# Optimization experiments

Measured on AMD Instinct MI355X. Metric: run time of the kernel, lower is better.

## Reference

```python
import jax, jax.numpy as jnp
import numpy as np

N = 100_000   # nodes
E = 1_600_000 # edges per relation (avg degree 16)
IN, H, O = 128, 128, 128


def _graph_conv(x, src, dst, W, b, relu):
    """DGL GraphConv, norm='both': y = D_dst^{-1/2} A D_src^{-1/2} x W + b."""
    ones = jnp.ones(src.shape[0], dtype=x.dtype)
    deg_out = jnp.clip(jax.ops.segment_sum(ones, src, num_segments=N), 1.0)  # [N]
    deg_in = jnp.clip(jax.ops.segment_sum(ones, dst, num_segments=N), 1.0)   # [N]
    h = (x * (deg_out ** -0.5)[:, None]) @ W                 # [N, out] transform first (in==out)
    agg = jax.ops.segment_sum(h[src], dst, num_segments=N)   # SpMM: gather + scatter-add
    y = agg * (deg_in ** -0.5)[:, None] + b
    return jax.nn.relu(y) if relu else y


def setup_inputs() -> dict:
    key = jax.random.key(0)
    ks = jax.random.split(key, 8)
    g = 0.1  # weight scale ~ xavier for d=128
    return {
        "x": jax.random.normal(ks[0], (N, IN), dtype=jnp.float32),
        "src_i": jax.random.randint(ks[1], (E,), 0, N),
        "dst_i": jax.random.randint(ks[2], (E,), 0, N),
        "src_b": jax.random.randint(ks[3], (E,), 0, N),
        "dst_b": jax.random.randint(ks[4], (E,), 0, N),
        "W1_i": jax.random.normal(ks[5], (IN, H), dtype=jnp.float32) * g,
        "b1_i": jnp.zeros((H,), dtype=jnp.float32),
        "W1_b": jax.random.normal(ks[6], (IN, H), dtype=jnp.float32) * g,
        "b1_b": jnp.zeros((H,), dtype=jnp.float32),
        "W2": jax.random.normal(ks[7], (H, O), dtype=jnp.float32) * g,
        "b2": jnp.zeros((O,), dtype=jnp.float32),
    }


def reference(x, src_i, dst_i, src_b, dst_b, W1_i, b1_i, W1_b, b1_b, W2, b2):
    # conv1: HeteroGraphConv({'interacts','behave'}, aggregate='sum'), ReLU inside each conv
    h = (_graph_conv(x, src_i, dst_i, W1_i, b1_i, relu=True)
         + _graph_conv(x, src_b, dst_b, W1_b, b1_b, relu=True))
    # conv2: only 'interacts', no activation
    return _graph_conv(h, src_i, dst_i, W2, b2, relu=False)
```

## Files before the change

kernel.cpp:

```cpp
#include <hip/hip_runtime.h>
#include <hip/hip_fp16.h>

#define N_NODES 100000
#define N_EDGES 1600000
#define XB 64
#define CHUNK (N_EDGES / XB)
#define HSH 2
#define HBINS (N_NODES / HSH)
#define PSH 128
#define PBINS ((N_NODES + PSH - 1) / PSH)
#define PCAP 16384
#define TILE 4096
#define WT_LD 136

typedef _Float16 half8_t __attribute__((ext_vector_type(8)));
typedef float f32x4 __attribute__((ext_vector_type(4)));
typedef unsigned long long u64;

__device__ inline unsigned packh2(float a, float b) {
  __half2 h = __floats2half2_rn(a, b);
  return *(unsigned*)&h;
}

__global__ __launch_bounds__(256) void k_hist(
    const int* __restrict__ src_i, const int* __restrict__ src_b,
    unsigned* __restrict__ part32) {
  __shared__ unsigned h[HBINS / 4];
  const int xb = blockIdx.x, job = blockIdx.y, sl = blockIdx.z;
  const int* arr = job ? src_b : src_i;
  const int lo = sl * HBINS;
  for (int i = threadIdx.x; i < HBINS / 4; i += 256) h[i] = 0;
  __syncthreads();
  const int4* a4 = (const int4*)(arr + xb * CHUNK);
  for (int q = threadIdx.x; q < CHUNK / 4; q += 256) {
    int4 v = a4[q];
    int t;
    t = v.x - lo; if ((unsigned)t < HBINS) atomicAdd(&h[t >> 2], 1u << ((t & 3) * 8));
    t = v.y - lo; if ((unsigned)t < HBINS) atomicAdd(&h[t >> 2], 1u << ((t & 3) * 8));
    t = v.z - lo; if ((unsigned)t < HBINS) atomicAdd(&h[t >> 2], 1u << ((t & 3) * 8));
    t = v.w - lo; if ((unsigned)t < HBINS) atomicAdd(&h[t >> 2], 1u << ((t & 3) * 8));
  }
  __syncthreads();
  unsigned* dst = part32 + ((size_t)(job * XB + xb) * N_NODES + lo) / 4;
  for (int i = threadIdx.x; i < HBINS / 4; i += 256) dst[i] = h[i];
}

__global__ __launch_bounds__(256) void k_hred(
    const unsigned* __restrict__ part32,
    float* __restrict__ dso_i, float* __restrict__ dso_b) {
  const int b4 = blockIdx.x * 256 + threadIdx.x;
  if (b4 >= N_NODES / 4) return;
  const int b0 = b4 * 4;
  const size_t Q = N_NODES / 4;
  int s0, s1, s2, s3;
  s0 = s1 = s2 = s3 = 0;
  for (int xb = 0; xb < XB; ++xb) {
    unsigned w = part32[(size_t)(0 * XB + xb) * Q + b4];
    s0 += w & 255; s1 += (w >> 8) & 255; s2 += (w >> 16) & 255; s3 += w >> 24;
  }
  dso_i[b0] = rsqrtf((float)max(s0, 1)); dso_i[b0 + 1] = rsqrtf((float)max(s1, 1));
  dso_i[b0 + 2] = rsqrtf((float)max(s2, 1)); dso_i[b0 + 3] = rsqrtf((float)max(s3, 1));
  s0 = s1 = s2 = s3 = 0;
  for (int xb = 0; xb < XB; ++xb) {
    unsigned w = part32[(size_t)(1 * XB + xb) * Q + b4];
    s0 += w & 255; s1 += (w >> 8) & 255; s2 += (w >> 16) & 255; s3 += w >> 24;
  }
  dso_b[b0] = rsqrtf((float)max(s0, 1)); dso_b[b0 + 1] = rsqrtf((float)max(s1, 1));
  dso_b[b0 + 2] = rsqrtf((float)max(s2, 1)); dso_b[b0 + 3] = rsqrtf((float)max(s3, 1));
}

__global__ __launch_bounds__(256) void k_bucket(
    const int* __restrict__ src_i, const int* __restrict__ dst_i,
    const int* __restrict__ src_b, const int* __restrict__ dst_b,
    int* __restrict__ bcur, unsigned* __restrict__ pairs) {
  __shared__ u64 stage[TILE];
  __shared__ int cnt[PSH], excl[PSH], gbase[PSH], lpos[PSH], sa[PSH], sb[PSH];
  const int rel = blockIdx.y;
  const int* src = rel ? src_b : src_i;
  const int* dst = rel ? dst_b : dst_i;
  const int tid = threadIdx.x;
  const int base = blockIdx.x * TILE;
  const int nE = min(TILE, N_EDGES - base);

  for (int i = tid; i < PSH; i += 256) { cnt[i] = 0; lpos[i] = 0; }
  __syncthreads();

  u64 ed[16];
  int eb[16];
#pragma unroll
  for (int j = 0; j < 16; ++j) {
    int idx = base + j * 256 + tid;
    if (idx < N_EDGES && (j * 256 + tid) < nE) {
      int s = src[idx], d = dst[idx];
      ed[j] = ((u64)(unsigned)d << 32) | (unsigned)s;
      eb[j] = d / PBINS;
      atomicAdd(&cnt[eb[j]], 1);
    } else {
      eb[j] = -1;
    }
  }
  __syncthreads();
  if (tid < PSH) sa[tid] = cnt[tid];
  __syncthreads();
  int* p = sa;
  int* q = sb;
  for (int d = 1; d < PSH; d <<= 1) {
    if (tid < PSH) q[tid] = ((tid >= d) ? p[tid - d] : 0) + p[tid];
    __syncthreads();
    int* tmp = p; p = q; q = tmp;
  }
  if (tid < PSH) {
    excl[tid] = p[tid] - cnt[tid];
    gbase[tid] = atomicAdd(&bcur[rel * PSH + tid], cnt[tid]);
  }
  __syncthreads();
#pragma unroll
  for (int j = 0; j < 16; ++j) {
    if (eb[j] >= 0) {
      int pos = excl[eb[j]] + atomicAdd(&lpos[eb[j]], 1);
      stage[pos] = ed[j];
    }
  }
  __syncthreads();
  for (int i = tid; i < nE; i += 256) {
    u64 e = stage[i];
    int d = (int)(e >> 32);
    int b = d / PBINS;
    unsigned pk = ((unsigned)(d - b * PBINS) << 17) | (unsigned)(e & 0x1FFFFu);
    pairs[(size_t)(rel * PSH + b) * PCAP + gbase[b] + (i - excl[b])] = pk;
  }
}

__global__ void k_bprefix(const int* __restrict__ bcur, int* __restrict__ bbase,
                          int* __restrict__ off_i, int* __restrict__ off_b) {
  __shared__ int ws[2][2];
  const int tid = threadIdx.x;
  const int rel = tid >> 7, i = tid & 127;
  const int lane = tid & 63;
  const int w2 = (tid >> 6) & 1;
  int v = bcur[rel * PSH + i];
  int x = v;
#pragma unroll
  for (int d = 1; d < 64; d <<= 1) {
    int t = __shfl_up(x, d);
    if (lane >= d) x += t;
  }
  if (lane == 63) ws[rel][w2] = x;
  __syncthreads();
  int addv = (w2 == 1) ? ws[rel][0] : 0;
  bbase[rel * PSH + i] = x - v + addv;
  if (tid == 0) { off_i[N_NODES] = N_EDGES; off_b[N_NODES] = N_EDGES; }
}

__global__ __launch_bounds__(256) void k_fill2(
    const int* __restrict__ bcur, const int* __restrict__ bbase,
    const unsigned* __restrict__ pairs,
    int* __restrict__ off_i, int* __restrict__ off_b,
    float* __restrict__ dsi_i, float* __restrict__ dsi_b,
    int* __restrict__ es_i, int* __restrict__ es_b) {
  __shared__ int cnt[PBINS];
  __shared__ int wsum[4];
  const int b = blockIdx.x, rel = blockIdx.y;
  const int lo = b * PBINS;
  const int hi = min(lo + PBINS, N_NODES);
  const int bins = hi - lo;
  int* off = rel ? off_b : off_i;
  float* dsi = rel ? dsi_b : dsi_i;
  int* es = rel ? es_b : es_i;
  const unsigned* seg = pairs + (size_t)(rel * PSH + b) * PCAP;
  const int nb = bcur[rel * PSH + b];
  const int base = bbase[rel * PSH + b];
  const int tid = threadIdx.x;
  for (int i = tid; i < bins; i += 256) cnt[i] = 0;
  __syncthreads();
  for (int i = tid; i < nb; i += 256) {
    int dl = (int)(seg[i] >> 17);
    atomicAdd(&cnt[dl], 1);
  }
  __syncthreads();
  const int i0 = tid * 4;
  int v[4];
#pragma unroll
  for (int k = 0; k < 4; ++k) v[k] = (i0 + k < bins) ? cnt[i0 + k] : 0;
  int tl = v[0] + v[1] + v[2] + v[3];
  const int lane = tid & 63, wid = tid >> 6;
  int x = tl;
#pragma unroll
  for (int d = 1; d < 64; d <<= 1) {
    int t = __shfl_up(x, d);
    if (lane >= d) x += t;
  }
  if (lane == 63) wsum[wid] = x;
  __syncthreads();
  int wb = 0;
#pragma unroll
  for (int w = 0; w < 4; ++w)
    if (w < wid) wb += wsum[w];
  int run = wb + x - tl;
#pragma unroll
  for (int k = 0; k < 4; ++k) {
    if (i0 + k < bins) {
      off[lo + i0 + k] = base + run;
      dsi[lo + i0 + k] = rsqrtf((float)max(v[k], 1));
      cnt[i0 + k] = run;
    }
    run += v[k];
  }
  __syncthreads();
  for (int i = tid; i < nb; i += 256) {
    unsigned e = seg[i];
    int dl = (int)(e >> 17);
    int p = atomicAdd(&cnt[dl], 1);
    es[base + p] = (int)(e & 0x1FFFFu);
  }
}

__global__ __launch_bounds__(256) void k_gemm_mfma(
    const float* __restrict__ A,
    const float* __restrict__ Wa, const float* __restrict__ Wb,
    const float* __restrict__ rsa, const float* __restrict__ rsb,
    unsigned short* __restrict__ Ca, unsigned short* __restrict__ Cb) {
  __shared__ unsigned short shw[128 * WT_LD];
  const int rel = blockIdx.y;
  const float* W = rel ? Wb : Wa;
  const float* rs = rel ? rsb : rsa;
  unsigned short* C = rel ? Cb : Ca;

  for (int t = threadIdx.x; t < 2048; t += 256) {
    int c4 = (t & 31) * 4;
    int k = (t >> 5) * 2;
    float4 w0 = *(const float4*)&W[k * 128 + c4];
    float4 w1 = *(const float4*)&W[(k + 1) * 128 + c4];
    *(unsigned*)&shw[(c4 + 0) * WT_LD + k] = packh2(w0.x, w1.x);
    *(unsigned*)&shw[(c4 + 1) * WT_LD + k] = packh2(w0.y, w1.y);
    *(unsigned*)&shw[(c4 + 2) * WT_LD + k] = packh2(w0.z, w1.z);
    *(unsigned*)&shw[(c4 + 3) * WT_LD + k] = packh2(w0.w, w1.w);
  }
  __syncthreads();

  const int w = threadIdx.x >> 6;
  const int l = threadIdx.x & 63;
  const int lc = l & 15;
  const int lk = l >> 4;
  const int rb = blockIdx.x * 128 + w * 32;

  f32x4 acc[2][8];
#pragma unroll
  for (int rf = 0; rf < 2; ++rf)
#pragma unroll
    for (int cf = 0; cf < 8; ++cf) acc[rf][cf] = (f32x4)(0.f);

  union H8 { unsigned u[4]; half8_t h; };

#pragma unroll
  for (int kc = 0; kc < 4; ++kc) {
    const int kbase = kc * 32 + lk * 8;
    H8 a[2];
#pragma unroll
    for (int rf = 0; rf < 2; ++rf) {
      int row = rb + rf * 16 + lc;
      row = min(row, N_NODES - 1);
      const float4* ap = (const float4*)(A + (size_t)row * 128 + kbase);
      float4 f0 = ap[0], f1 = ap[1];
      a[rf].u[0] = packh2(f0.x, f0.y);
      a[rf].u[1] = packh2(f0.z, f0.w);
      a[rf].u[2] = packh2(f1.x, f1.y);
      a[rf].u[3] = packh2(f1.z, f1.w);
    }
#pragma unroll
    for (int cf = 0; cf < 8; ++cf) {
      half8_t b = *(const half8_t*)&shw[(cf * 16 + lc) * WT_LD + kbase];
      acc[0][cf] = __builtin_amdgcn_mfma_f32_16x16x32_f16(a[0].h, b, acc[0][cf], 0, 0, 0);
      acc[1][cf] = __builtin_amdgcn_mfma_f32_16x16x32_f16(a[1].h, b, acc[1][cf], 0, 0, 0);
    }
  }

#pragma unroll
  for (int rf = 0; rf < 2; ++rf) {
#pragma unroll
    for (int reg = 0; reg < 4; ++reg) {
      int row = rb + rf * 16 + lk * 4 + reg;
      if (row < N_NODES) {
        float s = rs[row];
        unsigned short* crow = C + (size_t)row * 128 + lc;
#pragma unroll
        for (int cf = 0; cf < 8; ++cf) {
          __half h = __float2half_rn(acc[rf][cf][reg] * s);
          crow[cf * 16] = *(unsigned short*)&h;
        }
      }
    }
  }
}

__global__ __launch_bounds__(256) void k_gemm_mfma_h(
    const unsigned short* __restrict__ Ah,
    const float* __restrict__ W, const float* __restrict__ rs,
    unsigned short* __restrict__ C) {
  __shared__ unsigned short shw[128 * WT_LD];
  for (int t = threadIdx.x; t < 2048; t += 256) {
    int c4 = (t & 31) * 4;
    int k = (t >> 5) * 2;
    float4 w0 = *(const float4*)&W[k * 128 + c4];
    float4 w1 = *(const float4*)&W[(k + 1) * 128 + c4];
    *(unsigned*)&shw[(c4 + 0) * WT_LD + k] = packh2(w0.x, w1.x);
    *(unsigned*)&shw[(c4 + 1) * WT_LD + k] = packh2(w0.y, w1.y);
    *(unsigned*)&shw[(c4 + 2) * WT_LD + k] = packh2(w0.z, w1.z);
    *(unsigned*)&shw[(c4 + 3) * WT_LD + k] = packh2(w0.w, w1.w);
  }
  __syncthreads();

  const int w = threadIdx.x >> 6;
  const int l = threadIdx.x & 63;
  const int lc = l & 15;
  const int lk = l >> 4;
  const int rb = blockIdx.x * 128 + w * 32;

  f32x4 acc[2][8];
#pragma unroll
  for (int rf = 0; rf < 2; ++rf)
#pragma unroll
    for (int cf = 0; cf < 8; ++cf) acc[rf][cf] = (f32x4)(0.f);

#pragma unroll
  for (int kc = 0; kc < 4; ++kc) {
    const int kbase = kc * 32 + lk * 8;
    half8_t a[2];
#pragma unroll
    for (int rf = 0; rf < 2; ++rf) {
      int row = rb + rf * 16 + lc;
      row = min(row, N_NODES - 1);
      a[rf] = *(const half8_t*)&Ah[(size_t)row * 128 + kbase];
    }
#pragma unroll
    for (int cf = 0; cf < 8; ++cf) {
      half8_t b = *(const half8_t*)&shw[(cf * 16 + lc) * WT_LD + kbase];
      acc[0][cf] = __builtin_amdgcn_mfma_f32_16x16x32_f16(a[0], b, acc[0][cf], 0, 0, 0);
      acc[1][cf] = __builtin_amdgcn_mfma_f32_16x16x32_f16(a[1], b, acc[1][cf], 0, 0, 0);
    }
  }

#pragma unroll
  for (int rf = 0; rf < 2; ++rf) {
#pragma unroll
    for (int reg = 0; reg < 4; ++reg) {
      int row = rb + rf * 16 + lk * 4 + reg;
      if (row < N_NODES) {
        float s = rs[row];
        unsigned short* crow = C + (size_t)row * 128 + lc;
#pragma unroll
        for (int cf = 0; cf < 8; ++cf) {
          __half h = __float2half_rn(acc[rf][cf][reg] * s);
          crow[cf * 16] = *(unsigned short*)&h;
        }
      }
    }
  }
}

__device__ inline void spmm_acc(const uint4* __restrict__ Xv, const int* __restrict__ srcs,
                                int e0, int e1, int l, float* a) {
  int e = e0;
  for (; e + 16 <= e1; e += 16) {
    int s = srcs[e + l];
    uint4 v[16];
#pragma unroll
    for (int j = 0; j < 16; ++j) v[j] = Xv[(size_t)__shfl(s, j, 16) * 16 + l];
#pragma unroll
    for (int j = 0; j < 16; ++j) {
      float2 f;
      f = __half22float2(*(__half2*)&v[j].x); a[0] += f.x; a[1] += f.y;
      f = __half22float2(*(__half2*)&v[j].y); a[2] += f.x; a[3] += f.y;
      f = __half22float2(*(__half2*)&v[j].z); a[4] += f.x; a[5] += f.y;
      f = __half22float2(*(__half2*)&v[j].w); a[6] += f.x; a[7] += f.y;
    }
  }
  if (e < e1) {
    int s = (e + l < e1) ? srcs[e + l] : 0;
    int cnt = e1 - e;
    for (int j = 0; j < cnt; ++j) {
      uint4 v = Xv[(size_t)__shfl(s, j, 16) * 16 + l];
      float2 f;
      f = __half22float2(*(__half2*)&v.x); a[0] += f.x; a[1] += f.y;
      f = __half22float2(*(__half2*)&v.y); a[2] += f.x; a[3] += f.y;
      f = __half22float2(*(__half2*)&v.z); a[4] += f.x; a[5] += f.y;
      f = __half22float2(*(__half2*)&v.w); a[6] += f.x; a[7] += f.y;
    }
  }
}

__global__ __launch_bounds__(256) void k_spmm_l1(
    const unsigned short* __restrict__ Xi, const int* __restrict__ off_i,
    const int* __restrict__ es_i, const float* __restrict__ dsi_i,
    const float* __restrict__ b_i,
    const unsigned short* __restrict__ Xb, const int* __restrict__ off_b,
    const int* __restrict__ es_b, const float* __restrict__ dsi_b,
    const float* __restrict__ b_b, unsigned short* __restrict__ hout) {
  const int g = threadIdx.x >> 4;
  const int l = threadIdx.x & 15;
  const int n = blockIdx.x * 16 + g;
  if (n >= N_NODES) return;
  float y[8];
  {
    float a[8] = {0.f, 0.f, 0.f, 0.f, 0.f, 0.f, 0.f, 0.f};
    spmm_acc((const uint4*)Xi, es_i, off_i[n], off_i[n + 1], l, a);
    const float dn = dsi_i[n];
    float4 c0 = ((const float4*)b_i)[l * 2];
    float4 c1 = ((const float4*)b_i)[l * 2 + 1];
    y[0] = fmaxf(fmaf(a[0], dn, c0.x), 0.f); y[1] = fmaxf(fmaf(a[1], dn, c0.y), 0.f);
    y[2] = fmaxf(fmaf(a[2], dn, c0.z), 0.f); y[3] = fmaxf(fmaf(a[3], dn, c0.w), 0.f);
    y[4] = fmaxf(fmaf(a[4], dn, c1.x), 0.f); y[5] = fmaxf(fmaf(a[5], dn, c1.y), 0.f);
    y[6] = fmaxf(fmaf(a[6], dn, c1.z), 0.f); y[7] = fmaxf(fmaf(a[7], dn, c1.w), 0.f);
  }
  {
    float a[8] = {0.f, 0.f, 0.f, 0.f, 0.f, 0.f, 0.f, 0.f};
    spmm_acc((const uint4*)Xb, es_b, off_b[n], off_b[n + 1], l, a);
    const float dn = dsi_b[n];
    float4 c0 = ((const float4*)b_b)[l * 2];
    float4 c1 = ((const float4*)b_b)[l * 2 + 1];
    y[0] += fmaxf(fmaf(a[0], dn, c0.x), 0.f); y[1] += fmaxf(fmaf(a[1], dn, c0.y), 0.f);
    y[2] += fmaxf(fmaf(a[2], dn, c0.z), 0.f); y[3] += fmaxf(fmaf(a[3], dn, c0.w), 0.f);
    y[4] += fmaxf(fmaf(a[4], dn, c1.x), 0.f); y[5] += fmaxf(fmaf(a[5], dn, c1.y), 0.f);
    y[6] += fmaxf(fmaf(a[6], dn, c1.z), 0.f); y[7] += fmaxf(fmaf(a[7], dn, c1.w), 0.f);
  }
  uint4 hw;
  hw.x = packh2(y[0], y[1]);
  hw.y = packh2(y[2], y[3]);
  hw.z = packh2(y[4], y[5]);
  hw.w = packh2(y[6], y[7]);
  ((uint4*)hout)[(size_t)n * 16 + l] = hw;
}

__global__ __launch_bounds__(256) void k_spmm_l2(
    const unsigned short* __restrict__ Xh, const int* __restrict__ off,
    const int* __restrict__ srcs, const float* __restrict__ dsi,
    const float* __restrict__ bias, float* __restrict__ out) {
  const int g = threadIdx.x >> 4;
  const int l = threadIdx.x & 15;
  const int n = blockIdx.x * 16 + g;
  if (n >= N_NODES) return;
  float a[8] = {0.f, 0.f, 0.f, 0.f, 0.f, 0.f, 0.f, 0.f};
  spmm_acc((const uint4*)Xh, srcs, off[n], off[n + 1], l, a);
  const float dn = dsi[n];
  float4 c0 = ((const float4*)bias)[l * 2];
  float4 c1 = ((const float4*)bias)[l * 2 + 1];
  float4 y0, y1;
  y0.x = fmaf(a[0], dn, c0.x); y0.y = fmaf(a[1], dn, c0.y);
  y0.z = fmaf(a[2], dn, c0.z); y0.w = fmaf(a[3], dn, c0.w);
  y1.x = fmaf(a[4], dn, c1.x); y1.y = fmaf(a[5], dn, c1.y);
  y1.z = fmaf(a[6], dn, c1.z); y1.w = fmaf(a[7], dn, c1.w);
  float4* ov = (float4*)out;
  size_t oi = (size_t)n * 32 + l * 2;
  ov[oi] = y0;
  ov[oi + 1] = y1;
}

extern "C" void kernel_launch(void* const* d_in, const int* in_sizes, int n_in,
                              void* d_out, int out_size, void* d_ws, size_t ws_size,
                              hipStream_t stream) {
  const float* x    = (const float*)d_in[0];
  const int* src_i  = (const int*)d_in[1];
  const int* dst_i  = (const int*)d_in[2];
  const int* src_b  = (const int*)d_in[3];
  const int* dst_b  = (const int*)d_in[4];
  const float* W1_i = (const float*)d_in[5];
  const float* b1_i = (const float*)d_in[6];
  const float* W1_b = (const float*)d_in[7];
  const float* b1_b = (const float*)d_in[8];
  const float* W2   = (const float*)d_in[9];
  const float* b2   = (const float*)d_in[10];
  float* out = (float*)d_out;
  unsigned short* hbuf = (unsigned short*)d_out;

  char* ws = (char*)d_ws;
  size_t o = 0;
  auto alloc = [&](size_t bytes) {
    char* p = ws + o;
    o += (bytes + 255) & ~(size_t)255;
    return p;
  };
  float* dso_i = (float*)alloc(N_NODES * 4);
  float* dsi_i = (float*)alloc(N_NODES * 4);
  float* dso_b = (float*)alloc(N_NODES * 4);
  float* dsi_b = (float*)alloc(N_NODES * 4);
  int* off_i = (int*)alloc((N_NODES + 1) * 4);
  int* off_b = (int*)alloc((N_NODES + 1) * 4);
  int* bcur = (int*)alloc(2 * PSH * 4);
  int* bbase = (int*)alloc(2 * PSH * 4);
  int* es_i = (int*)alloc((size_t)N_EDGES * 4);
  int* es_b = (int*)alloc((size_t)N_EDGES * 4);
  char* uni = alloc((size_t)2 * N_NODES * 128 * 2);
  unsigned* part32      = (unsigned*)uni;
  unsigned* pairs       = (unsigned*)uni;
  unsigned short* buf_i = (unsigned short*)uni;
  unsigned short* buf_b = (unsigned short*)(uni + (size_t)N_NODES * 128 * 2);
  (void)ws_size; (void)in_sizes; (void)n_in; (void)out_size;

  hipMemsetAsync(bcur, 0, 2 * PSH * 4, stream);
  k_hist<<<dim3(XB, 2, HSH), dim3(256), 0, stream>>>(src_i, src_b, part32);
  k_hred<<<(N_NODES / 4 + 255) / 256, dim3(256), 0, stream>>>(part32, dso_i, dso_b);
  k_bucket<<<dim3((N_EDGES + TILE - 1) / TILE, 2), dim3(256), 0, stream>>>(
      src_i, dst_i, src_b, dst_b, bcur, pairs);
  k_bprefix<<<1, 256, 0, stream>>>(bcur, bbase, off_i, off_b);
  k_fill2<<<dim3(PSH, 2), dim3(256), 0, stream>>>(
      bcur, bbase, pairs, off_i, off_b, dsi_i, dsi_b, es_i, es_b);

  const int ggrid = (N_NODES + 127) / 128;
  const int sgrid = (N_NODES + 15) / 16;
  k_gemm_mfma<<<dim3(ggrid, 2), dim3(256), 0, stream>>>(
      x, W1_i, W1_b, dso_i, dso_b, buf_i, buf_b);
  k_spmm_l1<<<sgrid, 256, 0, stream>>>(
      buf_i, off_i, es_i, dsi_i, b1_i, buf_b, off_b, es_b, dsi_b, b1_b, hbuf);
  k_gemm_mfma_h<<<dim3(ggrid), dim3(256), 0, stream>>>(hbuf, W2, dso_i, buf_i);
  k_spmm_l2<<<sgrid, 256, 0, stream>>>(buf_i, off_i, es_i, dsi_i, b2, out);
}
```

Measured before the change: 456.1 us.

## Fold memset and bucket prefix into existing kernels, pack staging, merge GEMM relations

```diff
diff --git a/kernel.cpp b/kernel.cpp
--- a/kernel.cpp
+++ b/kernel.cpp
@@ -15,7 +15,6 @@
 
 typedef _Float16 half8_t __attribute__((ext_vector_type(8)));
 typedef float f32x4 __attribute__((ext_vector_type(4)));
-typedef unsigned long long u64;
 
 __device__ inline unsigned packh2(float a, float b) {
   __half2 h = __floats2half2_rn(a, b);
@@ -24,9 +23,10 @@
 
 __global__ __launch_bounds__(256) void k_hist(
     const int* __restrict__ src_i, const int* __restrict__ src_b,
-    unsigned* __restrict__ part32) {
+    unsigned* __restrict__ part32, int* __restrict__ bcur) {
   __shared__ unsigned h[HBINS / 4];
   const int xb = blockIdx.x, job = blockIdx.y, sl = blockIdx.z;
+  if (xb == 0 && job == 0 && sl == 0) bcur[threadIdx.x] = 0;
   const int* arr = job ? src_b : src_i;
   const int lo = sl * HBINS;
   for (int i = threadIdx.x; i < HBINS / 4; i += 256) h[i] = 0;
@@ -73,8 +73,9 @@
     const int* __restrict__ src_i, const int* __restrict__ dst_i,
     const int* __restrict__ src_b, const int* __restrict__ dst_b,
     int* __restrict__ bcur, unsigned* __restrict__ pairs) {
-  __shared__ u64 stage[TILE];
-  __shared__ int cnt[PSH], excl[PSH], gbase[PSH], lpos[PSH], sa[PSH], sb[PSH];
+  __shared__ unsigned stage[TILE];
+  __shared__ int cnt[PSH], gbase[PSH], lpos[PSH], sa[PSH], sb[PSH];
+  __shared__ int bnd[PSH + 1];
   const int rel = blockIdx.y;
   const int* src = rel ? src_b : src_i;
   const int* dst = rel ? dst_b : dst_i;
@@ -85,16 +86,17 @@
   for (int i = tid; i < PSH; i += 256) { cnt[i] = 0; lpos[i] = 0; }
   __syncthreads();
 
-  u64 ed[16];
+  unsigned pk[16];
   int eb[16];
 #pragma unroll
   for (int j = 0; j < 16; ++j) {
-    int idx = base + j * 256 + tid;
-    if (idx < N_EDGES && (j * 256 + tid) < nE) {
-      int s = src[idx], d = dst[idx];
-      ed[j] = ((u64)(unsigned)d << 32) | (unsigned)s;
-      eb[j] = d / PBINS;
-      atomicAdd(&cnt[eb[j]], 1);
+    int k = j * 256 + tid;
+    if (k < nE) {
+      int s = src[base + k], d = dst[base + k];
+      int b = d / PBINS;
+      pk[j] = ((unsigned)(d - b * PBINS) << 17) | (unsigned)s;
+      eb[j] = b;
+      atomicAdd(&cnt[b], 1);
     } else {
       eb[j] = -1;
     }
@@ -110,56 +112,39 @@
     int* tmp = p; p = q; q = tmp;
   }
   if (tid < PSH) {
-    excl[tid] = p[tid] - cnt[tid];
+    bnd[tid] = p[tid] - cnt[tid];
     gbase[tid] = atomicAdd(&bcur[rel * PSH + tid], cnt[tid]);
   }
+  if (tid == 0) bnd[PSH] = nE;
   __syncthreads();
 #pragma unroll
   for (int j = 0; j < 16; ++j) {
     if (eb[j] >= 0) {
-      int pos = excl[eb[j]] + atomicAdd(&lpos[eb[j]], 1);
-      stage[pos] = ed[j];
+      int pos = bnd[eb[j]] + atomicAdd(&lpos[eb[j]], 1);
+      stage[pos] = pk[j];
     }
   }
   __syncthreads();
   for (int i = tid; i < nE; i += 256) {
-    u64 e = stage[i];
-    int d = (int)(e >> 32);
-    int b = d / PBINS;
-    unsigned pk = ((unsigned)(d - b * PBINS) << 17) | (unsigned)(e & 0x1FFFFu);
-    pairs[(size_t)(rel * PSH + b) * PCAP + gbase[b] + (i - excl[b])] = pk;
-  }
-}
-
-__global__ void k_bprefix(const int* __restrict__ bcur, int* __restrict__ bbase,
-                          int* __restrict__ off_i, int* __restrict__ off_b) {
-  __shared__ int ws[2][2];
-  const int tid = threadIdx.x;
-  const int rel = tid >> 7, i = tid & 127;
-  const int lane = tid & 63;
-  const int w2 = (tid >> 6) & 1;
-  int v = bcur[rel * PSH + i];
-  int x = v;
-#pragma unroll
-  for (int d = 1; d < 64; d <<= 1) {
-    int t = __shfl_up(x, d);
-    if (lane >= d) x += t;
-  }
-  if (lane == 63) ws[rel][w2] = x;
-  __syncthreads();
-  int addv = (w2 == 1) ? ws[rel][0] : 0;
-  bbase[rel * PSH + i] = x - v + addv;
-  if (tid == 0) { off_i[N_NODES] = N_EDGES; off_b[N_NODES] = N_EDGES; }
+    int loB = 0, hiB = PSH;
+#pragma unroll
+    for (int it = 0; it < 7; ++it) {
+      int mid = (loB + hiB) >> 1;
+      if (bnd[mid] <= i) loB = mid; else hiB = mid;
+    }
+    pairs[(size_t)(rel * PSH + loB) * PCAP + gbase[loB] + (i - bnd[loB])] = stage[i];
+  }
 }
 
 __global__ __launch_bounds__(256) void k_fill2(
-    const int* __restrict__ bcur, const int* __restrict__ bbase,
-    const unsigned* __restrict__ pairs,
+    const int* __restrict__ bcur, const unsigned* __restrict__ pairs,
     int* __restrict__ off_i, int* __restrict__ off_b,
     float* __restrict__ dsi_i, float* __restrict__ dsi_b,
     int* __restrict__ es_i, int* __restrict__ es_b) {
   __shared__ int cnt[PBINS];
   __shared__ int wsum[4];
+  __shared__ int pb[PSH];
+  __shared__ int w0tot;
   const int b = blockIdx.x, rel = blockIdx.y;
   const int lo = b * PBINS;
   const int hi = min(lo + PBINS, N_NODES);
@@ -168,11 +153,28 @@
   float* dsi = rel ? dsi_b : dsi_i;
   int* es = rel ? es_b : es_i;
   const unsigned* seg = pairs + (size_t)(rel * PSH + b) * PCAP;
+  const int tid = threadIdx.x;
+  const int lane = tid & 63;
+
+  int bv = 0, bx = 0;
+  if (tid < PSH) {
+    bv = bcur[rel * PSH + tid];
+    bx = bv;
+#pragma unroll
+    for (int d = 1; d < 64; d <<= 1) {
+      int t = __shfl_up(bx, d);
+      if (lane >= d) bx += t;
+    }
+    if (tid == 63) w0tot = bx;
+  }
+  for (int i = tid; i < bins; i += 256) cnt[i] = 0;
+  __syncthreads();
+  if (tid < PSH) pb[tid] = bx - bv + ((tid >= 64) ? w0tot : 0);
+  __syncthreads();
   const int nb = bcur[rel * PSH + b];
-  const int base = bbase[rel * PSH + b];
-  const int tid = threadIdx.x;
-  for (int i = tid; i < bins; i += 256) cnt[i] = 0;
-  __syncthreads();
+  const int base = pb[b];
+  if (b == PSH - 1 && tid == 0) off[N_NODES] = N_EDGES;
+
   for (int i = tid; i < nb; i += 256) {
     int dl = (int)(seg[i] >> 17);
     atomicAdd(&cnt[dl], 1);
@@ -183,7 +185,7 @@
 #pragma unroll
   for (int k = 0; k < 4; ++k) v[k] = (i0 + k < bins) ? cnt[i0 + k] : 0;
   int tl = v[0] + v[1] + v[2] + v[3];
-  const int lane = tid & 63, wid = tid >> 6;
+  const int wid = tid >> 6;
   int x = tl;
 #pragma unroll
   for (int d = 1; d < 64; d <<= 1) {
@@ -215,78 +217,79 @@
   }
 }
 
-__global__ __launch_bounds__(256) void k_gemm_mfma(
+__global__ __launch_bounds__(256) void k_gemm12(
     const float* __restrict__ A,
     const float* __restrict__ Wa, const float* __restrict__ Wb,
     const float* __restrict__ rsa, const float* __restrict__ rsb,
     unsigned short* __restrict__ Ca, unsigned short* __restrict__ Cb) {
   __shared__ unsigned short shw[128 * WT_LD];
-  const int rel = blockIdx.y;
-  const float* W = rel ? Wb : Wa;
-  const float* rs = rel ? rsb : rsa;
-  unsigned short* C = rel ? Cb : Ca;
-
-  for (int t = threadIdx.x; t < 2048; t += 256) {
-    int c4 = (t & 31) * 4;
-    int k = (t >> 5) * 2;
-    float4 w0 = *(const float4*)&W[k * 128 + c4];
-    float4 w1 = *(const float4*)&W[(k + 1) * 128 + c4];
-    *(unsigned*)&shw[(c4 + 0) * WT_LD + k] = packh2(w0.x, w1.x);
-    *(unsigned*)&shw[(c4 + 1) * WT_LD + k] = packh2(w0.y, w1.y);
-    *(unsigned*)&shw[(c4 + 2) * WT_LD + k] = packh2(w0.z, w1.z);
-    *(unsigned*)&shw[(c4 + 3) * WT_LD + k] = packh2(w0.w, w1.w);
-  }
-  __syncthreads();
-
   const int w = threadIdx.x >> 6;
   const int l = threadIdx.x & 63;
   const int lc = l & 15;
   const int lk = l >> 4;
   const int rb = blockIdx.x * 128 + w * 32;
-
-  f32x4 acc[2][8];
-#pragma unroll
-  for (int rf = 0; rf < 2; ++rf)
-#pragma unroll
-    for (int cf = 0; cf < 8; ++cf) acc[rf][cf] = (f32x4)(0.f);
-
   union H8 { unsigned u[4]; half8_t h; };
 
-#pragma unroll
-  for (int kc = 0; kc < 4; ++kc) {
-    const int kbase = kc * 32 + lk * 8;
-    H8 a[2];
+  for (int rel = 0; rel < 2; ++rel) {
+    const float* W = rel ? Wb : Wa;
+    const float* rs = rel ? rsb : rsa;
+    unsigned short* C = rel ? Cb : Ca;
+
+    if (rel) __syncthreads();
+    for (int t = threadIdx.x; t < 2048; t += 256) {
+      int c4 = (t & 31) * 4;
+      int k = (t >> 5) * 2;
+      float4 w0 = *(const float4*)&W[k * 128 + c4];
+      float4 w1 = *(const float4*)&W[(k + 1) * 128 + c4];
+      *(unsigned*)&shw[(c4 + 0) * WT_LD + k] = packh2(w0.x, w1.x);
+      *(unsigned*)&shw[(c4 + 1) * WT_LD + k] = packh2(w0.y, w1.y);
+      *(unsigned*)&shw[(c4 + 2) * WT_LD + k] = packh2(w0.z, w1.z);
+      *(unsigned*)&shw[(c4 + 3) * WT_LD + k] = packh2(w0.w, w1.w);
+    }
+    __syncthreads();
+
+    f32x4 acc[2][8];
+#pragma unroll
+    for (int rf = 0; rf < 2; ++rf)
+#pragma unroll
+      for (int cf = 0; cf < 8; ++cf) acc[rf][cf] = (f32x4)(0.f);
+
+#pragma unroll
+    for (int kc = 0; kc < 4; ++kc) {
+      const int kbase = kc * 32 + lk * 8;
+      H8 a[2];
+#pragma unroll
+      for (int rf = 0; rf < 2; ++rf) {
+        int row = rb + rf * 16 + lc;
+        row = min(row, N_NODES - 1);
+        const float4* ap = (const float4*)(A + (size_t)row * 128 + kbase);
+        float4 f0 = ap[0], f1 = ap[1];
+        a[rf].u[0] = packh2(f0.x, f0.y);
+        a[rf].u[1] = packh2(f0.z, f0.w);
+        a[rf].u[2] = packh2(f1.x, f1.y);
+        a[rf].u[3] = packh2(f1.z, f1.w);
+      }
+#pragma unroll
+      for (int cf = 0; cf < 8; ++cf) {
+        half8_t b = *(const half8_t*)&shw[(cf * 16 + lc) * WT_LD + kbase];
+        acc[0][cf] = __builtin_amdgcn_mfma_f32_16x16x32_f16(a[0].h, b, acc[0][cf], 0, 0, 0);
+        acc[1][cf] = __builtin_amdgcn_mfma_f32_16x16x32_f16(a[1].h, b, acc[1][cf], 0, 0, 0);
+      }
+    }
+
 #pragma unroll
     for (int rf = 0; rf < 2; ++rf) {
-      int row = rb + rf * 16 + lc;
-      row = min(row, N_NODES - 1);
-      const float4* ap = (const float4*)(A + (size_t)row * 128 + kbase);
-      float4 f0 = ap[0], f1 = ap[1];
-      a[rf].u[0] = packh2(f0.x, f0.y);
-      a[rf].u[1] = packh2(f0.z, f0.w);
-      a[rf].u[2] = packh2(f1.x, f1.y);
-      a[rf].u[3] = packh2(f1.z, f1.w);
-    }
-#pragma unroll
-    for (int cf = 0; cf < 8; ++cf) {
-      half8_t b = *(const half8_t*)&shw[(cf * 16 + lc) * WT_LD + kbase];
-      acc[0][cf] = __builtin_amdgcn_mfma_f32_16x16x32_f16(a[0].h, b, acc[0][cf], 0, 0, 0);
-      acc[1][cf] = __builtin_amdgcn_mfma_f32_16x16x32_f16(a[1].h, b, acc[1][cf], 0, 0, 0);
-    }
-  }
-
-#pragma unroll
-  for (int rf = 0; rf < 2; ++rf) {
-#pragma unroll
-    for (int reg = 0; reg < 4; ++reg) {
-      int row = rb + rf * 16 + lk * 4 + reg;
-      if (row < N_NODES) {
-        float s = rs[row];
-        unsigned short* crow = C + (size_t)row * 128 + lc;
-#pragma unroll
-        for (int cf = 0; cf < 8; ++cf) {
-          __half h = __float2half_rn(acc[rf][cf][reg] * s);
-          crow[cf * 16] = *(unsigned short*)&h;
+#pragma unroll
+      for (int reg = 0; reg < 4; ++reg) {
+        int row = rb + rf * 16 + lk * 4 + reg;
+        if (row < N_NODES) {
+          float s = rs[row];
+          unsigned short* crow = C + (size_t)row * 128 + lc;
+#pragma unroll
+          for (int cf = 0; cf < 8; ++cf) {
+            __half h = __float2half_rn(acc[rf][cf][reg] * s);
+            crow[cf * 16] = *(unsigned short*)&h;
+          }
         }
       }
     }
@@ -486,7 +489,6 @@
   int* off_i = (int*)alloc((N_NODES + 1) * 4);
   int* off_b = (int*)alloc((N_NODES + 1) * 4);
   int* bcur = (int*)alloc(2 * PSH * 4);
-  int* bbase = (int*)alloc(2 * PSH * 4);
   int* es_i = (int*)alloc((size_t)N_EDGES * 4);
   int* es_b = (int*)alloc((size_t)N_EDGES * 4);
   char* uni = alloc((size_t)2 * N_NODES * 128 * 2);
@@ -496,18 +498,16 @@
   unsigned short* buf_b = (unsigned short*)(uni + (size_t)N_NODES * 128 * 2);
   (void)ws_size; (void)in_sizes; (void)n_in; (void)out_size;
 
-  hipMemsetAsync(bcur, 0, 2 * PSH * 4, stream);
-  k_hist<<<dim3(XB, 2, HSH), dim3(256), 0, stream>>>(src_i, src_b, part32);
+  k_hist<<<dim3(XB, 2, HSH), dim3(256), 0, stream>>>(src_i, src_b, part32, bcur);
   k_hred<<<(N_NODES / 4 + 255) / 256, dim3(256), 0, stream>>>(part32, dso_i, dso_b);
   k_bucket<<<dim3((N_EDGES + TILE - 1) / TILE, 2), dim3(256), 0, stream>>>(
       src_i, dst_i, src_b, dst_b, bcur, pairs);
-  k_bprefix<<<1, 256, 0, stream>>>(bcur, bbase, off_i, off_b);
   k_fill2<<<dim3(PSH, 2), dim3(256), 0, stream>>>(
-      bcur, bbase, pairs, off_i, off_b, dsi_i, dsi_b, es_i, es_b);
+      bcur, pairs, off_i, off_b, dsi_i, dsi_b, es_i, es_b);
 
   const int ggrid = (N_NODES + 127) / 128;
   const int sgrid = (N_NODES + 15) / 16;
-  k_gemm_mfma<<<dim3(ggrid, 2), dim3(256), 0, stream>>>(
+  k_gemm12<<<dim3(ggrid), dim3(256), 0, stream>>>(
       x, W1_i, W1_b, dso_i, dso_b, buf_i, buf_b);
   k_spmm_l1<<<sgrid, 256, 0, stream>>>(
       buf_i, off_i, es_i, dsi_i, b1_i, buf_b, off_b, es_b, dsi_b, b1_b, hbuf);
```

Result: no change. 458.2 us (+0.5%).
